# Optimization experiments

Hardware: AMD Instinct MI355X
Metric: run time of the kernel (lower is better)

## Reference

```python
import jax, jax.numpy as jnp
import numpy as np

K, P, Q, D = 16, 1024, 1024, 64  # heads, value-in dim, out dim, head dim; P'=P, Q'=Q, D'=D
B, N = 2, 2048                   # batch, seq (self-attention: M=N)
TEMPERATURE = jnp.sqrt(jnp.float32(D))

def _xavier(key, shape):
    fan_in, fan_out = shape[-2], shape[-1]
    lim = jnp.sqrt(6.0 / (fan_in + fan_out))
    return jax.random.uniform(key, shape, jnp.float32, -lim, lim)

def setup_inputs() -> dict:
    key = jax.random.key(0)
    k0, k1, k2, k3, k4 = jax.random.split(key, 5)
    return {
        'y_prime': jax.random.normal(k0, (B, N, Q), jnp.float32),
        'mask': jnp.zeros((N, N), jnp.float32),  # log-domain additive mask [M,N]
        'Lam_x': _xavier(k1, (K, P, D)),  # Lambda^(x): [K,P',D']
        'Lam_y': _xavier(k2, (K, Q, D)),  # Lambda^(y): [K,Q',D']
        'Th_x': _xavier(k3, (K, P, D)),   # Theta^(x):  [K,P,D]
        'Th_y': _xavier(k4, (K, Q, D)),   # Theta^(y):  [K,Q,D]
    }

def reference(y_prime, mask, Lam_x, Lam_y, Th_x, Th_y):
    # self-attention: x' = x = y'
    x_p = y_prime
    x = x_p
    # key projection: [B,M,K,D']
    r = jnp.einsum('bmp,kpd->bmkd', x_p, Lam_x)
    # bilinear scores: [K,B,M,N]
    r = jnp.einsum('bmkd,kqd,bnq->kbmn', r, Lam_y, y_prime)
    r = r + mask[None, None, :, :]
    # softmax over M (axis=-2), scaled by sqrt(D')
    A = jax.nn.softmax(r / TEMPERATURE, axis=-2)
    # value aggregation: [B,N,K,D]
    r = jnp.einsum('kbmn,bmp,kpd->bnkd', A, x, Th_x)
    # output projection: [B,N,Q]
    return jnp.einsum('bnkd,kqd->bnq', r, Th_y)
```

## Files before the change

### kernel.cpp

```cpp
#include <hip/hip_runtime.h>
#include <hip/hip_bf16.h>

#define KH 16
#define PD 1024
#define QD 1024
#define DD 64
#define BB 2
#define NN 2048
#define BN 4096
#define ST 72
#define SOFT_C 12.0f

typedef unsigned short u16;
typedef __attribute__((ext_vector_type(8))) short bf16x8;
typedef __attribute__((ext_vector_type(4))) short bf16x4;
typedef __attribute__((ext_vector_type(4))) float f32x4;

__device__ __forceinline__ float bf2f(u16 u) {
    return __uint_as_float(((unsigned)u) << 16);
}
__device__ __forceinline__ u16 f2bf(float f) {
    unsigned x = __float_as_uint(f);
    x += 0x7FFFu + ((x >> 16) & 1u);
    return (u16)(x >> 16);
}
__device__ __forceinline__ f32x4 mfma_k32(bf16x8 a, bf16x8 b, f32x4 c) {
    return __builtin_amdgcn_mfma_f32_16x16x32_bf16(a, b, c, 0, 0, 0);
}
__device__ __forceinline__ f32x4 mfma_k16(bf16x4 a, bf16x4 b, f32x4 c) {
#if __has_builtin(__builtin_amdgcn_mfma_f32_16x16x16bf16_1k)
    return __builtin_amdgcn_mfma_f32_16x16x16bf16_1k(a, b, c, 0, 0, 0);
#else
    asm("v_mfma_f32_16x16x16_bf16 %0, %1, %2, %0" : "+v"(c) : "v"(a), "v"(b));
    return c;
#endif
}
__device__ __forceinline__ bf16x8 ldfrag(const u16* base, int r0, int kc, int lane) {
    return *reinterpret_cast<const bf16x8*>(base + (r0 + (lane & 15)) * ST + kc +
                                            ((lane >> 4) << 3));
}
__device__ __forceinline__ bf16x4 ldfrag4(const u16* base, int r0, int kc, int lane) {
    return *reinterpret_cast<const bf16x4*>(base + (r0 + (lane & 15)) * ST + kc +
                                            ((lane >> 4) << 2));
}
__device__ __forceinline__ bf16x8 ldfragL(const u16* base, int r0, int kc, int lane) {
    return *reinterpret_cast<const bf16x8*>(base + ((r0 + (lane & 15)) << 6) + kc +
                                            ((lane >> 4) << 3));
}
__device__ __forceinline__ bf16x4 pack4(float a, float b, float c, float d) {
    union { bf16x4 v; __hip_bfloat162 h[2]; } u;
    u.h[0] = __float22bfloat162_rn(make_float2(a, b));
    u.h[1] = __float22bfloat162_rn(make_float2(c, d));
    return u.v;
}
__device__ __forceinline__ void gl_lds16(const u16* g, u16* l) {
    __builtin_amdgcn_global_load_lds(
        (const __attribute__((address_space(1))) void*)g,
        (__attribute__((address_space(3))) void*)l, 16, 0, 0);
}
template <int ROWS>
__device__ __forceinline__ void stage_dma(const u16* __restrict__ src, int ld,
                                          u16* dst, int lane, int w) {
#pragma unroll
    for (int c = 0; c < ROWS / 32; ++c) {
        int rbase = (w * (ROWS / 32) + c) * 8;
        const u16* g = src + (size_t)(rbase + (lane >> 3)) * ld + ((lane & 7) << 3);
        gl_lds16(g, dst + (rbase << 6));
    }
}
template <int ROWS, int NT>
__device__ __forceinline__ void stage_rows(const u16* __restrict__ src, int ld,
                                           u16* dst, int tid) {
#pragma unroll
    for (int it = 0; it < ROWS * 8 / NT; ++it) {
        int chunk = it * NT + tid;
        int row = chunk >> 3, col = (chunk & 7) << 3;
        *reinterpret_cast<uint4*>(dst + row * ST + col) =
            *reinterpret_cast<const uint4*>(src + row * ld + col);
    }
}

__global__ void detect_kernel(const u16* __restrict__ y, int* flag, int* mnz) {
    __shared__ int cnt;
    if (threadIdx.x == 0) cnt = 0;
    __syncthreads();
    int local = 0;
    for (int i = threadIdx.x; i < 8192; i += 256) {
        u16 u = y[i];
        int e = (u >> 7) & 0xFF;
        if (u == 0 || (e >= 96 && e < 160)) local++;
    }
    atomicAdd(&cnt, local);
    __syncthreads();
    if (threadIdx.x == 0) {
        *flag = (cnt > 7372) ? 1 : 0;
        *mnz = 0;
    }
}

__global__ __launch_bounds__(256) void prep_kernel(
    const void* __restrict__ ysrc, const void* __restrict__ msrc,
    const void* __restrict__ s0, const void* __restrict__ s1,
    const void* __restrict__ s2, const void* __restrict__ s3,
    u16* __restrict__ ycan, u16* __restrict__ LamXt, u16* __restrict__ LamYt,
    u16* __restrict__ ThXt, u16* __restrict__ ThYr, u16* __restrict__ maskc,
    const int* __restrict__ flag, int* __restrict__ mnz) {
    int z = blockIdx.z, bx = blockIdx.x, tid = threadIdx.x;
    int isbf = *flag;
    if (z == 0) {
        size_t n4 = (size_t)NN * NN / 8;
        if (!isbf) n4 *= 2;
        const uint4* p = (const uint4*)msrc;
        unsigned acc = 0;
        for (size_t i = (size_t)bx * 256 + tid; i < n4; i += 256 * 256) {
            uint4 v = p[i];
            acc |= v.x | v.y | v.z | v.w;
        }
        if (acc) atomicOr(mnz, 1);
    } else if (z == 1) {
        int n = BN * PD;
        for (int i = (bx * 256 + tid) * 4; i < n; i += 256 * 256 * 4) {
            if (isbf) {
                *reinterpret_cast<uint2*>(ycan + i) =
                    *reinterpret_cast<const uint2*>((const u16*)ysrc + i);
            } else {
                float4 f = *reinterpret_cast<const float4*>((const float*)ysrc + i);
                u16 t[4] = {f2bf(f.x), f2bf(f.y), f2bf(f.z), f2bf(f.w)};
                *reinterpret_cast<uint2*>(ycan + i) = *reinterpret_cast<uint2*>(t);
            }
        }
    } else if (z <= 4) {
        const void* src = (z == 2) ? s0 : (z == 3) ? s1 : s2;
        u16* dst = (z == 2) ? LamXt : (z == 3) ? LamYt : ThXt;
        float scale = (z == 3) ? 0.125f : 1.0f;
        int k = bx >> 4, p0 = (bx & 15) * 64;
        __shared__ float T[64][65];
        const u16* s16 = (const u16*)src + ((size_t)k * PD + p0) * DD;
        const float* s32 = (const float*)src + ((size_t)k * PD + p0) * DD;
#pragma unroll
        for (int it = 0; it < 2; ++it) {
            int chunk = it * 256 + tid;
            int row = chunk >> 3, c8 = (chunk & 7) << 3;
            float f[8];
            if (isbf) {
                uint4 v = *reinterpret_cast<const uint4*>(s16 + row * DD + c8);
                u16 t[8];
                *reinterpret_cast<uint4*>(t) = v;
#pragma unroll
                for (int e = 0; e < 8; ++e) f[e] = bf2f(t[e]);
            } else {
                float4 a = *reinterpret_cast<const float4*>(s32 + row * DD + c8);
                float4 b = *reinterpret_cast<const float4*>(s32 + row * DD + c8 + 4);
                f[0] = a.x; f[1] = a.y; f[2] = a.z; f[3] = a.w;
                f[4] = b.x; f[5] = b.y; f[6] = b.z; f[7] = b.w;
            }
#pragma unroll
            for (int e = 0; e < 8; ++e) T[row][c8 + e] = f[e] * scale;
        }
        __syncthreads();
        u16* drow = dst + (size_t)k * DD * PD + p0;
#pragma unroll
        for (int it = 0; it < 2; ++it) {
            int chunk = it * 256 + tid;
            int d = chunk >> 3, c8 = (chunk & 7) << 3;
            u16 t[8];
#pragma unroll
            for (int e = 0; e < 8; ++e) t[e] = f2bf(T[c8 + e][d]);
            *reinterpret_cast<uint4*>(drow + (size_t)d * PD + c8) =
                *reinterpret_cast<uint4*>(t);
        }
    } else if (z == 5) {
        int k = bx >> 4, q0 = (bx & 15) * 64;
#pragma unroll
        for (int it = 0; it < 2; ++it) {
            int chunk = it * 256 + tid;
            int row = chunk >> 3, c8 = (chunk & 7) << 3;
            size_t si = ((size_t)k * QD + q0 + row) * DD + c8;
            u16 t[8];
            if (isbf) {
                *reinterpret_cast<uint4*>(t) =
                    *reinterpret_cast<const uint4*>((const u16*)s3 + si);
            } else {
                float4 a = *reinterpret_cast<const float4*>((const float*)s3 + si);
                float4 b = *reinterpret_cast<const float4*>((const float*)s3 + si + 4);
                t[0] = f2bf(a.x); t[1] = f2bf(a.y); t[2] = f2bf(a.z); t[3] = f2bf(a.w);
                t[4] = f2bf(b.x); t[5] = f2bf(b.y); t[6] = f2bf(b.z); t[7] = f2bf(b.w);
            }
            *reinterpret_cast<uint4*>(ThYr + (size_t)(q0 + row) * (KH * DD) +
                                      k * DD + c8) = *reinterpret_cast<uint4*>(t);
        }
    } else {
        size_t n8 = (size_t)NN * NN / 8;
        for (size_t c = (size_t)bx * 256 + tid; c < n8; c += 256 * 256) {
            size_t i = c * 8;
            float f[8];
            if (isbf) {
                uint4 v = *reinterpret_cast<const uint4*>((const u16*)msrc + i);
                u16 t[8];
                *reinterpret_cast<uint4*>(t) = v;
#pragma unroll
                for (int e = 0; e < 8; ++e) f[e] = bf2f(t[e]);
            } else {
                float4 a = *reinterpret_cast<const float4*>((const float*)msrc + i);
                float4 b = *reinterpret_cast<const float4*>((const float*)msrc + i + 4);
                f[0] = a.x; f[1] = a.y; f[2] = a.z; f[3] = a.w;
                f[4] = b.x; f[5] = b.y; f[6] = b.z; f[7] = b.w;
            }
            u16 t[8];
#pragma unroll
            for (int e = 0; e < 8; ++e) t[e] = f2bf(f[e] * 0.125f);
            *reinterpret_cast<uint4*>(maskc + i) = *reinterpret_cast<uint4*>(t);
        }
    }
}

__global__ __launch_bounds__(256, 3) void proj_gemm(
    const u16* __restrict__ A,
    const u16* __restrict__ Bm,
    u16* __restrict__ Xk, u16* __restrict__ Yk, u16* __restrict__ Vtg) {
    int tid = threadIdx.x, lane = tid & 63, w = tid >> 6;
    int mhalf = w & 1, nhalf = w >> 1;
    int m0 = blockIdx.x * 128, n0 = blockIdx.y * 128;
    __shared__ u16 As[128 * 64];
    __shared__ u16 Bs[128 * 64];
    f32x4 acc[4][4] = {};

    for (int kk = 0; kk < PD; kk += 64) {
        __syncthreads();
        stage_dma<128>(A + (size_t)m0 * PD + kk, PD, As, lane, w);
        stage_dma<128>(Bm + (size_t)n0 * PD + kk, PD, Bs, lane, w);
        __syncthreads();
#pragma unroll
        for (int kc = 0; kc < 64; kc += 32) {
            bf16x8 af[4], bf[4];
#pragma unroll
            for (int i = 0; i < 4; ++i) af[i] = ldfragL(As, mhalf * 64 + i * 16, kc, lane);
#pragma unroll
            for (int j = 0; j < 4; ++j) bf[j] = ldfragL(Bs, nhalf * 64 + j * 16, kc, lane);
#pragma unroll
            for (int i = 0; i < 4; ++i)
#pragma unroll
                for (int j = 0; j < 4; ++j) acc[i][j] = mfma_k32(af[i], bf[j], acc[i][j]);
        }
    }
    int s = n0 >> 10;
    int quad = lane >> 4, col = lane & 15;
    u16* stg = nhalf ? Bs : As;
    __syncthreads();
    if (s == 2) {
#pragma unroll
        for (int i = 0; i < 4; ++i)
#pragma unroll
            for (int j = 0; j < 4; ++j)
                *reinterpret_cast<bf16x4*>(stg + (j * 16 + col) * 128 + mhalf * 64 +
                                           i * 16 + quad * 4) =
                    pack4(acc[i][j][0], acc[i][j][1], acc[i][j][2], acc[i][j][3]);
    } else {
#pragma unroll
        for (int i = 0; i < 4; ++i)
#pragma unroll
            for (int j = 0; j < 4; ++j)
#pragma unroll
                for (int reg = 0; reg < 4; ++reg)
                    stg[(mhalf * 64 + i * 16 + quad * 4 + reg) * 64 + j * 16 + col] =
                        f2bf(acc[i][j][reg]);
    }
    __syncthreads();
#pragma unroll
    for (int h = 0; h < 2; ++h) {
        int kh = ((n0 + h * 64) >> 6) & 15;
        const u16* src = h ? Bs : As;
        if (s == 2) {
            u16* vb = Vtg + (size_t)kh * DD * BN + m0;
#pragma unroll
            for (int it = 0; it < 4; ++it) {
                int chunk = it * 256 + tid;
                int d = chunk >> 4, off = (chunk & 15) * 8;
                *reinterpret_cast<uint4*>(vb + (size_t)d * BN + off) =
                    *reinterpret_cast<const uint4*>(src + d * 128 + off);
            }
        } else {
            u16* ob = (s == 0 ? Xk : Yk) + (size_t)kh * BN * DD + (size_t)m0 * DD;
#pragma unroll
            for (int it = 0; it < 4; ++it) {
                int chunk = it * 256 + tid;
                *reinterpret_cast<uint4*>(ob + chunk * 8) =
                    *reinterpret_cast<const uint4*>(src + chunk * 8);
            }
        }
    }
}

__global__ __launch_bounds__(512, 1) void attn_kernel(
    const u16* __restrict__ Xk,
    const u16* __restrict__ Yk,
    const u16* __restrict__ Vtg,
    const u16* __restrict__ maskc,
    const int* __restrict__ mnz,
    u16* __restrict__ O) {
    int tid = threadIdx.x, lane = tid & 63, w = tid >> 6;
    int quad = lane >> 4, col = lane & 15;
    int q0 = blockIdx.x * 128, k = blockIdx.y, b = blockIdx.z;
    const u16* Qp = Yk + ((size_t)k * BN + b * NN + q0) * DD;
    const u16* Kp = Xk + ((size_t)k * BN + b * NN) * DD;
    const u16* Vp = Vtg + (size_t)k * DD * BN + b * NN;
    __shared__ u16 Qs[128 * ST];
    __shared__ u16 Kb[3][64 * ST];
    __shared__ u16 Vb[3][64 * ST];
    int mz = *mnz;

    stage_rows<128, 512>(Qp, DD, Qs, tid);

    int srow = tid >> 3, scol = (tid & 7) << 3;
    const u16* kgp = Kp + (size_t)srow * DD + scol;
    const u16* vgp = Vp + (size_t)srow * BN + scol;
    int soff = srow * ST + scol;

    uint4 kr = *reinterpret_cast<const uint4*>(kgp);
    uint4 vr = *reinterpret_cast<const uint4*>(vgp);
    *reinterpret_cast<uint4*>(Kb[0] + soff) = kr;
    *reinterpret_cast<uint4*>(Vb[0] + soff) = vr;
    kr = *reinterpret_cast<const uint4*>(kgp + (size_t)64 * DD);
    vr = *reinterpret_cast<const uint4*>(vgp + 64);
    __syncthreads();

    bf16x8 qf0 = ldfrag(Qs, w * 16, 0, lane);
    bf16x8 qf1 = ldfrag(Qs, w * 16, 32, lane);

    float lp = 0.0f;
    f32x4 oacc[4] = {};

    for (int t = 0; t < 32; ++t) {
        int cur = t % 3;
        if (t < 31) {
            int nxt = (t + 1) % 3;
            *reinterpret_cast<uint4*>(Kb[nxt] + soff) = kr;
            *reinterpret_cast<uint4*>(Vb[nxt] + soff) = vr;
            if (t < 30) {
                kr = *reinterpret_cast<const uint4*>(kgp + (size_t)(t + 2) * 64 * DD);
                vr = *reinterpret_cast<const uint4*>(vgp + (t + 2) * 64);
            }
            __syncthreads();
        }
        const u16* Ks = Kb[cur];
        const u16* Vt = Vb[cur];
        int m0 = t * 64;

        f32x4 sacc[4] = {};
#pragma unroll
        for (int kg = 0; kg < 4; ++kg) {
            bf16x8 a0 = ldfrag(Ks, kg * 16, 0, lane);
            bf16x8 a1 = ldfrag(Ks, kg * 16, 32, lane);
            sacc[kg] = mfma_k32(a0, qf0, sacc[kg]);
            sacc[kg] = mfma_k32(a1, qf1, sacc[kg]);
        }
        if (mz) {
#pragma unroll
            for (int kg = 0; kg < 4; ++kg)
#pragma unroll
                for (int reg = 0; reg < 4; ++reg)
                    sacc[kg][reg] += bf2f(
                        maskc[(size_t)(m0 + kg * 16 + quad * 4 + reg) * NN + q0 +
                              w * 16 + col]);
        }
        bf16x4 pb[4];
#pragma unroll
        for (int kg = 0; kg < 4; ++kg) {
            float p0 = __expf(sacc[kg][0] - SOFT_C);
            float p1 = __expf(sacc[kg][1] - SOFT_C);
            float p2 = __expf(sacc[kg][2] - SOFT_C);
            float p3 = __expf(sacc[kg][3] - SOFT_C);
            lp += (p0 + p1) + (p2 + p3);
            pb[kg] = pack4(p0, p1, p2, p3);
        }
#pragma unroll
        for (int kg = 0; kg < 4; ++kg)
#pragma unroll
            for (int dg = 0; dg < 4; ++dg) {
                bf16x4 av = ldfrag4(Vt, dg * 16, kg * 16, lane);
                oacc[dg] = mfma_k16(av, pb[kg], oacc[dg]);
            }
    }

    float l = lp;
    l += __shfl_xor(l, 16);
    l += __shfl_xor(l, 32);
    float inv = 1.0f / l;

#pragma unroll
    for (int dg = 0; dg < 4; ++dg)
        *reinterpret_cast<bf16x4*>(Qs + (w * 16 + col) * ST + dg * 16 + quad * 4) =
            pack4(oacc[dg][0] * inv, oacc[dg][1] * inv, oacc[dg][2] * inv,
                  oacc[dg][3] * inv);
    __syncthreads();
#pragma unroll
    for (int it = 0; it < 2; ++it) {
        int chunk = it * 512 + tid;
        int row = chunk >> 3, c8 = (chunk & 7) << 3;
        *reinterpret_cast<uint4*>(O + (size_t)(b * NN + q0 + row) * (KH * DD) +
                                  k * DD + c8) =
            *reinterpret_cast<const uint4*>(Qs + row * ST + c8);
    }
}

__global__ __launch_bounds__(256, 3) void out_gemm(
    const u16* __restrict__ A,
    const u16* __restrict__ Bm,
    const int* __restrict__ flag,
    void* __restrict__ outv) {
    int tid = threadIdx.x, lane = tid & 63, w = tid >> 6;
    int mhalf = w & 1, nhalf = w >> 1;
    int m0 = blockIdx.x * 128, n0 = blockIdx.y * 128;
    __shared__ u16 S[2][128 * 64];
    u16* As = S[0];
    u16* Bs = S[1];
    f32x4 acc[4][4] = {};

    for (int kk = 0; kk < KH * DD; kk += 64) {
        __syncthreads();
        stage_dma<128>(A + (size_t)m0 * (KH * DD) + kk, KH * DD, As, lane, w);
        stage_dma<128>(Bm + (size_t)n0 * (KH * DD) + kk, KH * DD, Bs, lane, w);
        __syncthreads();
#pragma unroll
        for (int kc = 0; kc < 64; kc += 32) {
            bf16x8 af[4], bf[4];
#pragma unroll
            for (int i = 0; i < 4; ++i) af[i] = ldfragL(As, mhalf * 64 + i * 16, kc, lane);
#pragma unroll
            for (int j = 0; j < 4; ++j) bf[j] = ldfragL(Bs, nhalf * 64 + j * 16, kc, lane);
#pragma unroll
            for (int i = 0; i < 4; ++i)
#pragma unroll
                for (int j = 0; j < 4; ++j) acc[i][j] = mfma_k32(af[i], bf[j], acc[i][j]);
        }
    }
    int isbf = *flag;
    int quad = lane >> 4, col = lane & 15;
    if (isbf) {
#pragma unroll
        for (int i = 0; i < 4; ++i)
#pragma unroll
            for (int j = 0; j < 4; ++j)
#pragma unroll
                for (int reg = 0; reg < 4; ++reg) {
                    size_t row = m0 + mhalf * 64 + i * 16 + quad * 4 + reg;
                    int c = n0 + nhalf * 64 + j * 16 + col;
                    ((u16*)outv)[row * QD + c] = f2bf(acc[i][j][reg]);
                }
    } else {
        float* Sf = (float*)&S[0][0];
#pragma unroll
        for (int h = 0; h < 2; ++h) {
            __syncthreads();
            if (mhalf == h) {
#pragma unroll
                for (int i = 0; i < 4; ++i)
#pragma unroll
                    for (int j = 0; j < 4; ++j)
#pragma unroll
                        for (int reg = 0; reg < 4; ++reg)
                            Sf[(i * 16 + quad * 4 + reg) * 128 + nhalf * 64 +
                               j * 16 + col] = acc[i][j][reg];
            }
            __syncthreads();
            float* orow = (float*)outv + (size_t)(m0 + h * 64) * QD + n0;
#pragma unroll
            for (int it = 0; it < 8; ++it) {
                int chunk = it * 256 + tid;
                int row = chunk >> 5, c4 = (chunk & 31) * 4;
                *reinterpret_cast<float4*>(orow + (size_t)row * QD + c4) =
                    *reinterpret_cast<const float4*>(Sf + row * 128 + c4);
            }
        }
    }
}

extern "C" void kernel_launch(void* const* d_in, const int* in_sizes, int n_in,
                              void* d_out, int out_size, void* d_ws, size_t ws_size,
                              hipStream_t stream) {
    char* wsb = (char*)d_ws;
    int* flag = (int*)wsb;
    int* mnz = (int*)(wsb + 16);
    u16* ycan = (u16*)(wsb + 64);
    const size_t NYP = (size_t)BN * PD;
    const size_t NW = (size_t)KH * PD * DD;
    const size_t OSZ = (size_t)BN * KH * DD;
    u16* Wcat = ycan + NYP;
    u16* ThYr = Wcat + 3 * NW;
    u16* Xk = ThYr + NW;
    u16* Yk = Xk + OSZ;
    u16* Vtg = Yk + OSZ;
    u16* maskc = Vtg + OSZ;
    u16* Ob = ycan;

    detect_kernel<<<1, 256, 0, stream>>>((const u16*)d_in[0], flag, mnz);
    prep_kernel<<<dim3(256, 1, 7), 256, 0, stream>>>(
        d_in[0], d_in[1], d_in[2], d_in[3], d_in[4], d_in[5], ycan, Wcat,
        Wcat + NW, Wcat + 2 * NW, ThYr, maskc, flag, mnz);
    proj_gemm<<<dim3(BN / 128, 3072 / 128), 256, 0, stream>>>(ycan, Wcat, Xk, Yk, Vtg);
    attn_kernel<<<dim3(NN / 128, KH, BB), 512, 0, stream>>>(Xk, Yk, Vtg, maskc,
                                                            mnz, Ob);
    out_gemm<<<dim3(BN / 128, QD / 128), 256, 0, stream>>>(Ob, ThYr, flag, d_out);
}
```

Baseline: 237.8 us.

## Split attention waves by KV-tile parity, widen query tiles, use K32 MFMA for PV

```diff
diff --git a/kernel.cpp b/kernel.cpp
--- a/kernel.cpp
+++ b/kernel.cpp
@@ -10,6 +10,8 @@
 #define BN 4096
 #define ST 72
 #define SOFT_C 12.0f
+#define LOG2E 1.4426950408889634f
+#define SOFT_C2 17.312340490667560f
 
 typedef unsigned short u16;
 typedef __attribute__((ext_vector_type(8))) short bf16x8;
@@ -26,14 +28,6 @@
 }
 __device__ __forceinline__ f32x4 mfma_k32(bf16x8 a, bf16x8 b, f32x4 c) {
     return __builtin_amdgcn_mfma_f32_16x16x32_bf16(a, b, c, 0, 0, 0);
-}
-__device__ __forceinline__ f32x4 mfma_k16(bf16x4 a, bf16x4 b, f32x4 c) {
-#if __has_builtin(__builtin_amdgcn_mfma_f32_16x16x16bf16_1k)
-    return __builtin_amdgcn_mfma_f32_16x16x16bf16_1k(a, b, c, 0, 0, 0);
-#else
-    asm("v_mfma_f32_16x16x16_bf16 %0, %1, %2, %0" : "+v"(c) : "v"(a), "v"(b));
-    return c;
-#endif
 }
 __device__ __forceinline__ bf16x8 ldfrag(const u16* base, int r0, int kc, int lane) {
     return *reinterpret_cast<const bf16x8*>(base + (r0 + (lane & 15)) * ST + kc +
@@ -66,17 +60,6 @@
         int rbase = (w * (ROWS / 32) + c) * 8;
         const u16* g = src + (size_t)(rbase + (lane >> 3)) * ld + ((lane & 7) << 3);
         gl_lds16(g, dst + (rbase << 6));
-    }
-}
-template <int ROWS, int NT>
-__device__ __forceinline__ void stage_rows(const u16* __restrict__ src, int ld,
-                                           u16* dst, int tid) {
-#pragma unroll
-    for (int it = 0; it < ROWS * 8 / NT; ++it) {
-        int chunk = it * NT + tid;
-        int row = chunk >> 3, col = (chunk & 7) << 3;
-        *reinterpret_cast<uint4*>(dst + row * ST + col) =
-            *reinterpret_cast<const uint4*>(src + row * ld + col);
     }
 }
 
@@ -291,7 +274,7 @@
     }
 }
 
-__global__ __launch_bounds__(512, 1) void attn_kernel(
+__global__ __launch_bounds__(512, 4) void attn_kernel(
     const u16* __restrict__ Xk,
     const u16* __restrict__ Yk,
     const u16* __restrict__ Vtg,
@@ -300,16 +283,24 @@
     u16* __restrict__ O) {
     int tid = threadIdx.x, lane = tid & 63, w = tid >> 6;
     int quad = lane >> 4, col = lane & 15;
+    int par = w >> 2;
+    int wq = w & 3;
     int q0 = blockIdx.x * 128, k = blockIdx.y, b = blockIdx.z;
     const u16* Qp = Yk + ((size_t)k * BN + b * NN + q0) * DD;
     const u16* Kp = Xk + ((size_t)k * BN + b * NN) * DD;
     const u16* Vp = Vtg + (size_t)k * DD * BN + b * NN;
-    __shared__ u16 Qs[128 * ST];
-    __shared__ u16 Kb[3][64 * ST];
-    __shared__ u16 Vb[3][64 * ST];
+    __shared__ u16 smem[2 * 3 * 64 * ST];
+    u16* Kb0 = smem;
+    u16* Vb0 = smem + 3 * 64 * ST;
     int mz = *mnz;
 
-    stage_rows<128, 512>(Qp, DD, Qs, tid);
+    bf16x8 qf[2][2];
+#pragma unroll
+    for (int qg = 0; qg < 2; ++qg) {
+        const u16* qrow = Qp + (size_t)(wq * 32 + qg * 16 + col) * DD + (quad << 3);
+        qf[qg][0] = *reinterpret_cast<const bf16x8*>(qrow);
+        qf[qg][1] = *reinterpret_cast<const bf16x8*>(qrow + 32);
+    }
 
     int srow = tid >> 3, scol = (tid & 7) << 3;
     const u16* kgp = Kp + (size_t)srow * DD + scol;
@@ -318,80 +309,122 @@
 
     uint4 kr = *reinterpret_cast<const uint4*>(kgp);
     uint4 vr = *reinterpret_cast<const uint4*>(vgp);
-    *reinterpret_cast<uint4*>(Kb[0] + soff) = kr;
-    *reinterpret_cast<uint4*>(Vb[0] + soff) = vr;
+    *reinterpret_cast<uint4*>(Kb0 + soff) = kr;
+    *reinterpret_cast<uint4*>(Vb0 + soff) = vr;
     kr = *reinterpret_cast<const uint4*>(kgp + (size_t)64 * DD);
     vr = *reinterpret_cast<const uint4*>(vgp + 64);
     __syncthreads();
 
-    bf16x8 qf0 = ldfrag(Qs, w * 16, 0, lane);
-    bf16x8 qf1 = ldfrag(Qs, w * 16, 32, lane);
-
-    float lp = 0.0f;
-    f32x4 oacc[4] = {};
+    float lp[2] = {0.0f, 0.0f};
+    f32x4 oacc[4][2] = {};
 
     for (int t = 0; t < 32; ++t) {
         int cur = t % 3;
         if (t < 31) {
             int nxt = (t + 1) % 3;
-            *reinterpret_cast<uint4*>(Kb[nxt] + soff) = kr;
-            *reinterpret_cast<uint4*>(Vb[nxt] + soff) = vr;
+            *reinterpret_cast<uint4*>(Kb0 + nxt * (64 * ST) + soff) = kr;
+            *reinterpret_cast<uint4*>(Vb0 + nxt * (64 * ST) + soff) = vr;
             if (t < 30) {
                 kr = *reinterpret_cast<const uint4*>(kgp + (size_t)(t + 2) * 64 * DD);
                 vr = *reinterpret_cast<const uint4*>(vgp + (t + 2) * 64);
             }
             __syncthreads();
         }
-        const u16* Ks = Kb[cur];
-        const u16* Vt = Vb[cur];
+        if ((t & 1) != par) continue;
+        const u16* Ks = Kb0 + cur * (64 * ST);
+        const u16* Vt = Vb0 + cur * (64 * ST);
         int m0 = t * 64;
 
-        f32x4 sacc[4] = {};
+        bf16x4 pb4[4][2];
 #pragma unroll
         for (int kg = 0; kg < 4; ++kg) {
             bf16x8 a0 = ldfrag(Ks, kg * 16, 0, lane);
             bf16x8 a1 = ldfrag(Ks, kg * 16, 32, lane);
-            sacc[kg] = mfma_k32(a0, qf0, sacc[kg]);
-            sacc[kg] = mfma_k32(a1, qf1, sacc[kg]);
-        }
-        if (mz) {
-#pragma unroll
-            for (int kg = 0; kg < 4; ++kg)
-#pragma unroll
-                for (int reg = 0; reg < 4; ++reg)
-                    sacc[kg][reg] += bf2f(
-                        maskc[(size_t)(m0 + kg * 16 + quad * 4 + reg) * NN + q0 +
-                              w * 16 + col]);
-        }
-        bf16x4 pb[4];
-#pragma unroll
-        for (int kg = 0; kg < 4; ++kg) {
-            float p0 = __expf(sacc[kg][0] - SOFT_C);
-            float p1 = __expf(sacc[kg][1] - SOFT_C);
-            float p2 = __expf(sacc[kg][2] - SOFT_C);
-            float p3 = __expf(sacc[kg][3] - SOFT_C);
-            lp += (p0 + p1) + (p2 + p3);
-            pb[kg] = pack4(p0, p1, p2, p3);
-        }
-#pragma unroll
-        for (int kg = 0; kg < 4; ++kg)
+#pragma unroll
+            for (int qg = 0; qg < 2; ++qg) {
+                f32x4 s = {};
+                s = mfma_k32(a0, qf[qg][0], s);
+                s = mfma_k32(a1, qf[qg][1], s);
+                if (mz) {
+#pragma unroll
+                    for (int reg = 0; reg < 4; ++reg)
+                        s[reg] += bf2f(
+                            maskc[(size_t)(m0 + kg * 16 + quad * 4 + reg) * NN +
+                                  q0 + wq * 32 + qg * 16 + col]);
+                }
+                float p0 = exp2f(fmaf(s[0], LOG2E, -SOFT_C2));
+                float p1 = exp2f(fmaf(s[1], LOG2E, -SOFT_C2));
+                float p2 = exp2f(fmaf(s[2], LOG2E, -SOFT_C2));
+                float p3 = exp2f(fmaf(s[3], LOG2E, -SOFT_C2));
+                lp[qg] += (p0 + p1) + (p2 + p3);
+                pb4[kg][qg] = pack4(p0, p1, p2, p3);
+            }
+        }
+#pragma unroll
+        for (int half = 0; half < 2; ++half) {
+            bf16x8 pb8[2];
+#pragma unroll
+            for (int qg = 0; qg < 2; ++qg)
+                pb8[qg] = __builtin_shufflevector(pb4[half * 2][qg],
+                                                  pb4[half * 2 + 1][qg],
+                                                  0, 1, 2, 3, 4, 5, 6, 7);
 #pragma unroll
             for (int dg = 0; dg < 4; ++dg) {
-                bf16x4 av = ldfrag4(Vt, dg * 16, kg * 16, lane);
-                oacc[dg] = mfma_k16(av, pb[kg], oacc[dg]);
-            }
-    }
-
-    float l = lp;
-    l += __shfl_xor(l, 16);
-    l += __shfl_xor(l, 32);
-    float inv = 1.0f / l;
-
-#pragma unroll
-    for (int dg = 0; dg < 4; ++dg)
-        *reinterpret_cast<bf16x4*>(Qs + (w * 16 + col) * ST + dg * 16 + quad * 4) =
-            pack4(oacc[dg][0] * inv, oacc[dg][1] * inv, oacc[dg][2] * inv,
-                  oacc[dg][3] * inv);
+                bf16x4 v0 = ldfrag4(Vt, dg * 16, half * 32, lane);
+                bf16x4 v1 = ldfrag4(Vt, dg * 16, half * 32 + 16, lane);
+                bf16x8 av = __builtin_shufflevector(v0, v1, 0, 1, 2, 3, 4, 5, 6, 7);
+#pragma unroll
+                for (int qg = 0; qg < 2; ++qg)
+                    oacc[dg][qg] = mfma_k32(av, pb8[qg], oacc[dg][qg]);
+            }
+        }
+    }
+
+    __syncthreads();
+    float* red = (float*)smem;
+    const int RS = 66;
+    if (par == 1) {
+#pragma unroll
+        for (int qg = 0; qg < 2; ++qg) {
+            float l2 = lp[qg];
+            l2 += __shfl_xor(l2, 16);
+            l2 += __shfl_xor(l2, 32);
+            int q = wq * 32 + qg * 16 + col;
+            if (quad == 0) red[q * RS + 64] = l2;
+#pragma unroll
+            for (int dg = 0; dg < 4; ++dg) {
+                *reinterpret_cast<float2*>(red + q * RS + dg * 16 + quad * 4) =
+                    make_float2(oacc[dg][qg][0], oacc[dg][qg][1]);
+                *reinterpret_cast<float2*>(red + q * RS + dg * 16 + quad * 4 + 2) =
+                    make_float2(oacc[dg][qg][2], oacc[dg][qg][3]);
+            }
+        }
+    }
+    __syncthreads();
+    u16* Ost = smem + 2 * 3 * 64 * ST - 128 * ST;
+    if (par == 0) {
+#pragma unroll
+        for (int qg = 0; qg < 2; ++qg) {
+            int q = wq * 32 + qg * 16 + col;
+            float l2 = lp[qg];
+            l2 += __shfl_xor(l2, 16);
+            l2 += __shfl_xor(l2, 32);
+            l2 += red[q * RS + 64];
+            float inv = 1.0f / l2;
+#pragma unroll
+            for (int dg = 0; dg < 4; ++dg) {
+                float2 r0 = *reinterpret_cast<const float2*>(red + q * RS + dg * 16 +
+                                                             quad * 4);
+                float2 r1 = *reinterpret_cast<const float2*>(red + q * RS + dg * 16 +
+                                                             quad * 4 + 2);
+                *reinterpret_cast<bf16x4*>(Ost + q * ST + dg * 16 + quad * 4) =
+                    pack4((oacc[dg][qg][0] + r0.x) * inv,
+                          (oacc[dg][qg][1] + r0.y) * inv,
+                          (oacc[dg][qg][2] + r1.x) * inv,
+                          (oacc[dg][qg][3] + r1.y) * inv);
+            }
+        }
+    }
     __syncthreads();
 #pragma unroll
     for (int it = 0; it < 2; ++it) {
@@ -399,7 +432,7 @@
         int row = chunk >> 3, c8 = (chunk & 7) << 3;
         *reinterpret_cast<uint4*>(O + (size_t)(b * NN + q0 + row) * (KH * DD) +
                                   k * DD + c8) =
-            *reinterpret_cast<const uint4*>(Qs + row * ST + c8);
+            *reinterpret_cast<const uint4*>(Ost + row * ST + c8);
     }
 }
 
```

Result: no change. 237.3 us (-0.2%).
